# Kernel optimization log

Measured on AMD Instinct MI355X. Metric: run time of the kernel, lower is better.

## Reference

```python
import jax, jax.numpy as jnp
import numpy as np

B, N, P, K = 4, 512, 1024, 20
LMAX, SH_DIM, MUL, NB = 2, 9, 64, 20
CUT, T, NSPEC = 4.0, 3, 119
E = N * K
PE = P * K
L_SLICES = [(0, 1), (1, 4), (4, 9)]


def spherical_harmonics(vec):
    # component-normalized real SH up to l=2 on the unit vector (e3nn 'component' norm: ||Y_l||^2 = 2l+1)
    r = jnp.sqrt(jnp.sum(vec * vec, axis=-1, keepdims=True))
    u = vec / jnp.maximum(r, 1e-9)
    x, y, z = u[:, 0], u[:, 1], u[:, 2]
    s3, s5, s15 = 3.0 ** 0.5, 5.0 ** 0.5, 15.0 ** 0.5
    return jnp.stack([
        jnp.ones_like(x),
        s3 * x, s3 * y, s3 * z,
        s15 * x * y, s15 * y * z, 0.5 * s5 * (3.0 * z * z - 1.0),
        s15 * x * z, 0.5 * s15 * (x * x - y * y),
    ], axis=-1)  # [E, 9]


def radial_basis(r):
    # gaussian RBF, centers linspace(0, cutoff, num_basis)
    centers = jnp.linspace(0.0, CUT, NB)
    sigma = CUT / NB
    return jnp.exp(-((r[:, None] - centers[None, :]) / sigma) ** 2)


def per_l_linear(a, Wl):
    # a: [n, 9, mul]; Wl: [3, mul, mul]; independent channel-mixing per angular momentum l
    return jnp.concatenate([a[:, s:e, :] @ Wl[l] for l, (s, e) in enumerate(L_SLICES)], axis=1)


def conv_layer(h_src_feats, sh, rbf, src, dst, n_out, Wr1, br1, Wr2, br2, Wl, Wg):
    # radial MLP -> per-edge weights; gather scalar source features; tensor-product-style message sh (x) (w*s)
    w = jax.nn.silu(rbf @ Wr1 + br1) @ Wr2 + br2                 # [E, mul]
    s_src = h_src_feats[src, 0, :]                               # [E, mul]
    m = sh[:, :, None] * (s_src * w)[:, None, :]                 # [E, 9, mul]
    a = jax.ops.segment_sum(m, dst, num_segments=n_out) / (K ** 0.5)
    u = per_l_linear(a, Wl)                                      # [n, 9, mul]
    gate = jax.nn.sigmoid(a[:, 0, :] @ Wg)                       # gate activation for l>0
    return jnp.concatenate([jax.nn.silu(u[:, :1, :]), u[:, 1:, :] * gate[:, None, :]], axis=1)


def _forward(atom_xyz, atom_edges_displacement, cell, probe_xyz, probe_edges_displacement,
             W_embed, Wr1, br1, Wr2, br2, Wl, Wg,
             pWr1, pbr1, pWr2, pbr2, pWl, pWg, W_out,
             atom_edges, probe_edges, nodes):
    Na, Np, Et, PEt = B * N, B * P, B * E, B * PE
    pos = atom_xyz.reshape(Na, 3)          # unpad_and_cat with uniform lengths == reshape
    ppos = probe_xyz.reshape(Np, 3)
    node_off = (jnp.arange(B, dtype=atom_edges.dtype) * N)[:, None, None]
    a_edges = (atom_edges + node_off).reshape(Et, 2)
    p_off = jnp.concatenate([node_off, (jnp.arange(B, dtype=atom_edges.dtype) * P)[:, None, None]], axis=2)
    p_edges = (probe_edges + p_off).reshape(PEt, 2)
    # fractional displacement -> cartesian via per-graph cell (repeat_interleave over edges)
    cell_a = jnp.repeat(cell, E, axis=0)
    cell_p = jnp.repeat(cell, PE, axis=0)
    disp_a = jnp.einsum('ei,eij->ej', atom_edges_displacement.reshape(Et, 3), cell_a)
    disp_p = jnp.einsum('ei,eij->ej', probe_edges_displacement.reshape(PEt, 3), cell_p)
    src, dst = a_edges[:, 0], a_edges[:, 1]
    edge_vec = pos[dst] - (pos[src] + disp_a)
    sh = spherical_harmonics(edge_vec)
    rbf = radial_basis(jnp.linalg.norm(edge_vec, axis=1))
    psrc, pdst = p_edges[:, 0], p_edges[:, 1]
    p_vec = ppos[pdst] - (pos[psrc] + disp_p)
    psh = spherical_harmonics(p_vec)
    prbf = radial_basis(jnp.linalg.norm(p_vec, axis=1))
    # AtomicConfigurationModel: one-hot species -> scalar channel, T interaction layers, keep per-layer reps
    onehot = jax.nn.one_hot(nodes.reshape(Na), NSPEC, dtype=W_embed.dtype)
    h = jnp.zeros((Na, SH_DIM, MUL), W_embed.dtype).at[:, 0, :].set(onehot @ W_embed)
    reps = []
    for t in range(T):
        h = h + conv_layer(h, sh, rbf, src, dst, Na, Wr1[t], br1[t], Wr2[t], br2[t], Wl[t], Wg[t])
        reps.append(h)
    # AtomicPotentialModel: atom->probe message passing using per-layer atom representations
    p = jnp.zeros((Np, SH_DIM, MUL), W_embed.dtype)
    for t in range(T):
        p = p + conv_layer(reps[t], psh, prbf, psrc, pdst, Np, pWr1[t], pbr1[t], pWr2[t], pbr2[t], pWl[t], pWg[t])
    out = (p[:, 0, :] @ W_out)[:, 0].reshape(B, P)  # readout to 0e scalar, pad_and_stack == reshape
    return out


def setup_inputs():
    key = jax.random.key(0)
    ks = jax.random.split(key, 20)
    f32 = jnp.float32
    atom_xyz = jax.random.uniform(ks[0], (B, N, 3), f32) * 8.0
    probe_xyz = jax.random.uniform(ks[1], (B, P, 3), f32) * 8.0
    cell = jnp.tile(jnp.eye(3, dtype=f32)[None] * 8.0, (B, 1, 1))
    atom_edges = jax.random.randint(ks[2], (B, E, 2), 0, N, jnp.int32)
    probe_edges = jnp.concatenate([
        jax.random.randint(ks[3], (B, PE, 1), 0, N, jnp.int32),
        jax.random.randint(ks[4], (B, PE, 1), 0, P, jnp.int32)], axis=2)
    atom_edges_displacement = jax.random.randint(ks[5], (B, E, 3), -1, 2).astype(f32)
    probe_edges_displacement = jax.random.randint(ks[6], (B, PE, 3), -1, 2).astype(f32)
    nodes = jax.random.randint(ks[7], (B, N), 1, 84, jnp.int32)
    num_nodes = jnp.full((B,), N, jnp.int32)
    num_atom_edges = jnp.full((B,), E, jnp.int32)
    num_probes = jnp.full((B,), P, jnp.int32)
    num_probe_edges = jnp.full((B,), PE, jnp.int32)
    rn = lambda k, s: jax.random.normal(k, s, f32) * 0.1
    W_embed = rn(ks[8], (NSPEC, MUL))
    Wr1 = rn(ks[9], (T, NB, 100)); br1 = jnp.zeros((T, 100), f32)
    Wr2 = rn(ks[10], (T, 100, MUL)); br2 = jnp.zeros((T, MUL), f32)
    Wl = rn(ks[11], (T, 3, MUL, MUL)); Wg = rn(ks[12], (T, MUL, MUL))
    pWr1 = rn(ks[13], (T, NB, 100)); pbr1 = jnp.zeros((T, 100), f32)
    pWr2 = rn(ks[14], (T, 100, MUL)); pbr2 = jnp.zeros((T, MUL), f32)
    pWl = rn(ks[15], (T, 3, MUL, MUL)); pWg = rn(ks[16], (T, MUL, MUL))
    W_out = rn(ks[17], (MUL, 1))
    return dict(atom_xyz=atom_xyz, atom_edges_displacement=atom_edges_displacement, cell=cell,
                probe_xyz=probe_xyz, probe_edges_displacement=probe_edges_displacement,
                W_embed=W_embed, Wr1=Wr1, br1=br1, Wr2=Wr2, br2=br2, Wl=Wl, Wg=Wg,
                pWr1=pWr1, pbr1=pbr1, pWr2=pWr2, pbr2=pbr2, pWl=pWl, pWg=pWg, W_out=W_out,
                atom_edges=atom_edges, probe_edges=probe_edges, nodes=nodes,
                num_nodes=num_nodes, num_atom_edges=num_atom_edges,
                num_probes=num_probes, num_probe_edges=num_probe_edges)


def reference(atom_xyz, atom_edges_displacement, cell, probe_xyz, probe_edges_displacement,
              W_embed, Wr1, br1, Wr2, br2, Wl, Wg,
              pWr1, pbr1, pWr2, pbr2, pWl, pWg, W_out,
              atom_edges, probe_edges, nodes, num_nodes, num_atom_edges, num_probes, num_probe_edges):
    # num_* are uniform (all graphs same size); unpad_and_cat reduces to reshape.
    return _forward(atom_xyz, atom_edges_displacement, cell, probe_xyz, probe_edges_displacement,
                    W_embed, Wr1, br1, Wr2, br2, Wl, Wg,
                    pWr1, pbr1, pWr2, pbr2, pWl, pWg, W_out,
                    atom_edges, probe_edges, nodes)
```

## Files before the change

### kernel.cpp

```cpp
#include <hip/hip_runtime.h>
#include <math.h>

#define Bc 4
#define Nc 512
#define Pc 1024
#define Kc 20
#define MUL 64
#define NBc 20
#define HID 100
#define Tc 3
#define CUTc 4.0f
#define Ec (Nc * Kc)
#define PEc (Pc * Kc)
#define NA (Bc * Nc)
#define NP (Bc * Pc)
#define ET (Bc * Ec)
#define PET (Bc * PEc)
#define TBL 1024
#define RMAXT 5.25f
#define CAP 64
#define TROWS 8
#define TBLOCKS (6 * TBL / TROWS)
#define ZBLOCKS 8
#define EBLOCKS 32

__device__ __forceinline__ float silu_f(float x) { return x / (1.0f + __expf(-x)); }
__device__ __forceinline__ float lane_bcast_f(float v, int l) {
    return __int_as_float(__builtin_amdgcn_readlane(__float_as_int(v), l));
}

__global__ __launch_bounds__(256) void front_kernel(
    const float* __restrict__ Wr1, const float* __restrict__ pWr1,
    const float* __restrict__ br1, const float* __restrict__ pbr1,
    const float* __restrict__ Wr2, const float* __restrict__ pWr2,
    const float* __restrict__ br2, const float* __restrict__ pbr2,
    const int* __restrict__ nodes, const float* __restrict__ Wemb,
    int* __restrict__ cnt_both, float* __restrict__ h0row,
    float* __restrict__ wtab)
{
    __shared__ float Hs[TROWS * HID];
    int bid = blockIdx.x;
    int t = threadIdx.x;

    if (bid < TBLOCKS) {
        int grow0 = bid * TROWS;
        int ly = grow0 / TBL;
        int t3 = (ly < 3) ? ly : ly - 3;
        const float* w1 = ((ly < 3) ? Wr1 : pWr1) + (size_t)t3 * NBc * HID;
        const float* b1 = ((ly < 3) ? br1 : pbr1) + (size_t)t3 * HID;
        const float* w2 = ((ly < 3) ? Wr2 : pWr2) + (size_t)t3 * HID * MUL;
        const float* b2 = ((ly < 3) ? br2 : pbr2) + (size_t)t3 * MUL;
        const float step = CUTc / (NBc - 1);
        const float inv_sigma = (float)NBc / CUTc;

        for (int id = t; id < TROWS * HID; id += 256) {
            int il = id / HID, j = id - il * HID;
            float r = (float)(grow0 % TBL + il) * (RMAXT / (float)TBL);
            float s = b1[j];
#pragma unroll
            for (int k = 0; k < NBc; ++k) {
                float tt = (r - k * step) * inv_sigma;
                s = fmaf(__expf(-tt * tt), w1[k * HID + j], s);
            }
            Hs[id] = silu_f(s);
        }
        __syncthreads();

        int il0 = t >> 6, c = t & 63;
        for (int il = il0; il < TROWS; il += 4) {
            float acc = b2[c];
#pragma unroll 4
            for (int j = 0; j < HID; ++j)
                acc = fmaf(Hs[il * HID + j], w2[(size_t)j * MUL + c], acc);
            wtab[(size_t)(grow0 + il) * MUL + c] = acc;
        }
    } else if (bid < TBLOCKS + ZBLOCKS) {
        int idx = (bid - TBLOCKS) * 256 + t;
        for (int i = idx; i < NA + NP; i += ZBLOCKS * 256) cnt_both[i] = 0;
    } else {
        int idx = (bid - TBLOCKS - ZBLOCKS) * 256 + t;
        for (int i = idx; i < NA * MUL; i += EBLOCKS * 256) {
            int a = i >> 6, c = i & 63;
            h0row[i] = Wemb[nodes[a] * MUL + c];
        }
    }
}

__global__ void geom_kernel(const float* __restrict__ apos,
                            const float* __restrict__ ppos,
                            const int* __restrict__ a_edges,
                            const int* __restrict__ p_edges,
                            const float* __restrict__ a_disp,
                            const float* __restrict__ p_disp,
                            const float* __restrict__ cell,
                            int* __restrict__ cnt_a, int* __restrict__ cnt_p,
                            float* __restrict__ br_a, int* __restrict__ bs_a,
                            float* __restrict__ br_p, int* __restrict__ bs_p)
{
    int e = blockIdx.x * 256 + threadIdx.x;
    if (e >= ET + PET) return;
    const int* edges; const float* displ; const float* pdst;
    int* cnt; float* brout; int* bsout;
    int el, Eper, dst_stride;
    if (e < ET) {
        el = e; edges = a_edges; displ = a_disp; pdst = apos;
        Eper = Ec; dst_stride = Nc; cnt = cnt_a; brout = br_a; bsout = bs_a;
    } else {
        el = e - ET; edges = p_edges; displ = p_disp; pdst = ppos;
        Eper = PEc; dst_stride = Pc; cnt = cnt_p; brout = br_p; bsout = bs_p;
    }
    int b = el / Eper;
    int sg = edges[el * 2 + 0] + b * Nc;
    int dg = edges[el * 2 + 1] + b * dst_stride;
    const float* C = cell + b * 9;
    float d0 = displ[el * 3 + 0], d1 = displ[el * 3 + 1], d2 = displ[el * 3 + 2];
    float dx = d0 * C[0] + d1 * C[3] + d2 * C[6];
    float dy = d0 * C[1] + d1 * C[4] + d2 * C[7];
    float dz = d0 * C[2] + d1 * C[5] + d2 * C[8];
    float vx = pdst[dg * 3 + 0] - (apos[sg * 3 + 0] + dx);
    float vy = pdst[dg * 3 + 1] - (apos[sg * 3 + 1] + dy);
    float vz = pdst[dg * 3 + 2] - (apos[sg * 3 + 2] + dz);
    float r = sqrtf(vx * vx + vy * vy + vz * vz);
    int pos = atomicAdd(&cnt[dg], 1);
    if (pos < CAP) {
        brout[(size_t)dg * CAP + pos] = r;
        bsout[(size_t)dg * CAP + pos] = sg;
    }
}

__global__ __launch_bounds__(256) void layer_kernel(
    const float* __restrict__ hsrc,
    float* __restrict__ outb,
    const int* __restrict__ cnt,
    const float* __restrict__ brk, const int* __restrict__ bsk,
    const float* __restrict__ wtab,
    const float* __restrict__ Wl0)
{
    __shared__ float tile[4][64];
    int c = threadIdx.x & 63;
    int w = threadIdx.x >> 6;
    int n = blockIdx.x * 4 + w;

    int m = min(cnt[n], CAP);
    float rvec = 0.0f; int svec = 0;
    if (c < m) { rvec = brk[(size_t)n * CAP + c]; svec = bsk[(size_t)n * CAP + c]; }
    float acc = 0.0f;
    const float scale = (float)TBL / RMAXT;
#pragma unroll 4
    for (int p = 0; p < m; ++p) {
        float rr = lane_bcast_f(rvec, p);
        int sg = __builtin_amdgcn_readlane(svec, p);
        float x = fminf(rr * scale, (float)TBL - 1.001f);
        int i0 = (int)x;
        float f = x - (float)i0;
        const float* tp = wtab + (size_t)i0 * MUL;
        float w0 = tp[c];
        float w1 = tp[MUL + c];
        float wv = fmaf(w1 - w0, f, w0);
        acc = fmaf(hsrc[(size_t)sg * MUL + c], wv, acc);
    }
    acc *= 0.22360679774997896f;

    tile[w][c] = acc;
    float u = 0.0f;
#pragma unroll
    for (int k4 = 0; k4 < 16; ++k4) {
        float4 av = *(const float4*)&tile[w][k4 * 4];
        u = fmaf(av.x, Wl0[(k4 * 4 + 0) * 64 + c], u);
        u = fmaf(av.y, Wl0[(k4 * 4 + 1) * 64 + c], u);
        u = fmaf(av.z, Wl0[(k4 * 4 + 2) * 64 + c], u);
        u = fmaf(av.w, Wl0[(k4 * 4 + 3) * 64 + c], u);
    }
    outb[(size_t)n * MUL + c] = hsrc[(size_t)n * MUL + c] + silu_f(u);
}

__global__ __launch_bounds__(256) void probe3_kernel(
    const float* __restrict__ rep0, const float* __restrict__ rep1,
    const float* __restrict__ rep2,
    const int* __restrict__ cnt,
    const float* __restrict__ brk, const int* __restrict__ bsk,
    const float* __restrict__ wtab,
    const float* __restrict__ pWl,
    const float* __restrict__ Wout,
    float* __restrict__ out)
{
    __shared__ float tile[4][64];
    int c = threadIdx.x & 63;
    int w = threadIdx.x >> 6;
    int n = blockIdx.x * 4 + w;

    int m = min(cnt[n], CAP);
    float rvec = 0.0f; int svec = 0;
    if (c < m) { rvec = brk[(size_t)n * CAP + c]; svec = bsk[(size_t)n * CAP + c]; }
    float acc0 = 0.0f, acc1 = 0.0f, acc2 = 0.0f;
    const float scale = (float)TBL / RMAXT;
    const float* wt0 = wtab;
    const float* wt1 = wtab + (size_t)TBL * MUL;
    const float* wt2 = wtab + (size_t)2 * TBL * MUL;
#pragma unroll 2
    for (int p = 0; p < m; ++p) {
        float rr = lane_bcast_f(rvec, p);
        int sg = __builtin_amdgcn_readlane(svec, p);
        float x = fminf(rr * scale, (float)TBL - 1.001f);
        int i0 = (int)x;
        float f = x - (float)i0;
        size_t rowo = (size_t)i0 * MUL + c;
        float wv0 = fmaf(wt0[rowo + MUL] - wt0[rowo], f, wt0[rowo]);
        float wv1 = fmaf(wt1[rowo + MUL] - wt1[rowo], f, wt1[rowo]);
        float wv2 = fmaf(wt2[rowo + MUL] - wt2[rowo], f, wt2[rowo]);
        size_t so = (size_t)sg * MUL + c;
        acc0 = fmaf(rep0[so], wv0, acc0);
        acc1 = fmaf(rep1[so], wv1, acc1);
        acc2 = fmaf(rep2[so], wv2, acc2);
    }
    const float isk = 0.22360679774997896f;
    float res = 0.0f;
    float accs[3] = {acc0, acc1, acc2};
#pragma unroll
    for (int t = 0; t < 3; ++t) {
        tile[w][c] = accs[t] * isk;
        const float* W = pWl + (size_t)t * 3 * MUL * MUL;
        float u = 0.0f;
#pragma unroll
        for (int k4 = 0; k4 < 16; ++k4) {
            float4 av = *(const float4*)&tile[w][k4 * 4];
            u = fmaf(av.x, W[(k4 * 4 + 0) * 64 + c], u);
            u = fmaf(av.y, W[(k4 * 4 + 1) * 64 + c], u);
            u = fmaf(av.z, W[(k4 * 4 + 2) * 64 + c], u);
            u = fmaf(av.w, W[(k4 * 4 + 3) * 64 + c], u);
        }
        res += silu_f(u);
    }

    float v = res * Wout[c];
#pragma unroll
    for (int o = 32; o > 0; o >>= 1) v += __shfl_down(v, o, 64);
    if (c == 0) out[n] = v;
}

extern "C" void kernel_launch(void* const* d_in, const int* in_sizes, int n_in,
                              void* d_out, int out_size, void* d_ws, size_t ws_size,
                              hipStream_t stream)
{
    const float* atom_xyz  = (const float*)d_in[0];
    const float* a_disp    = (const float*)d_in[1];
    const float* cell      = (const float*)d_in[2];
    const float* probe_xyz = (const float*)d_in[3];
    const float* p_disp    = (const float*)d_in[4];
    const float* W_embed   = (const float*)d_in[5];
    const float* Wr1       = (const float*)d_in[6];
    const float* br1       = (const float*)d_in[7];
    const float* Wr2       = (const float*)d_in[8];
    const float* br2       = (const float*)d_in[9];
    const float* Wl        = (const float*)d_in[10];
    const float* pWr1      = (const float*)d_in[12];
    const float* pbr1      = (const float*)d_in[13];
    const float* pWr2      = (const float*)d_in[14];
    const float* pbr2      = (const float*)d_in[15];
    const float* pWl       = (const float*)d_in[16];
    const float* W_out     = (const float*)d_in[18];
    const int*   atom_edges  = (const int*)d_in[19];
    const int*   probe_edges = (const int*)d_in[20];
    const int*   nodes       = (const int*)d_in[21];
    float* out = (float*)d_out;

    char* w = (char*)d_ws;
    auto alloc = [&](size_t bytes) -> void* {
        void* r = (void*)w;
        w += (bytes + 255) & ~(size_t)255;
        return r;
    };
    int*   cnt_both = (int*)alloc((size_t)(NA + NP) * 4);
    int*   cnt_a  = cnt_both;
    int*   cnt_p  = cnt_both + NA;
    float* br_a   = (float*)alloc((size_t)NA * CAP * 4);
    int*   bs_a   = (int*)alloc((size_t)NA * CAP * 4);
    float* br_p   = (float*)alloc((size_t)NP * CAP * 4);
    int*   bs_p   = (int*)alloc((size_t)NP * CAP * 4);
    float* h0row  = (float*)alloc((size_t)NA * MUL * 4);
    float* rep0   = (float*)alloc((size_t)NA * MUL * 4);
    float* rep1   = (float*)alloc((size_t)NA * MUL * 4);
    float* rep2   = (float*)alloc((size_t)NA * MUL * 4);
    float* wtab   = (float*)alloc((size_t)6 * TBL * MUL * 4);

    front_kernel<<<TBLOCKS + ZBLOCKS + EBLOCKS, 256, 0, stream>>>(
        Wr1, pWr1, br1, pbr1, Wr2, pWr2, br2, pbr2,
        nodes, W_embed, cnt_both, h0row, wtab);

    geom_kernel<<<(ET + PET + 255) / 256, 256, 0, stream>>>(
        atom_xyz, probe_xyz, atom_edges, probe_edges, a_disp, p_disp, cell,
        cnt_a, cnt_p, br_a, bs_a, br_p, bs_p);

    const float* hprev = h0row;
    float* reps[3] = {rep0, rep1, rep2};
    for (int t = 0; t < Tc; ++t) {
        layer_kernel<<<NA / 4, 256, 0, stream>>>(
            hprev, reps[t], cnt_a, br_a, bs_a,
            wtab + (size_t)t * TBL * MUL,
            Wl + (size_t)t * 3 * MUL * MUL);
        hprev = reps[t];
    }

    probe3_kernel<<<NP / 4, 256, 0, stream>>>(
        rep0, rep1, rep2, cnt_p, br_p, bs_p,
        wtab + (size_t)3 * TBL * MUL, pWl, W_out, out);
}
```

Before: 77.30 us.

## Interleave per-layer probe convolutions with atom layer launches in a combined kernel

Replaces the separate atom layer kernels and the single three-layer probe kernel with one kernel that runs atom-layer blocks and probe-layer blocks side by side. Probe interaction t now runs in the same launch as atom layer t+1, so probe work fills the GPU while the atom chain proceeds. The probe results are accumulated across launches in a new per-probe buffer with a phase flag. This adds a global read and write of that buffer per probe, and it gives up the single probe pass that reused the same edge list for all three layers.

Result: no change. 76.82 us (-0.6%).

```diff
diff --git a/kernel.cpp b/kernel.cpp
--- a/kernel.cpp
+++ b/kernel.cpp
@@ -128,114 +128,98 @@
     }
 }
 
-__global__ __launch_bounds__(256) void layer_kernel(
-    const float* __restrict__ hsrc,
-    float* __restrict__ outb,
-    const int* __restrict__ cnt,
-    const float* __restrict__ brk, const int* __restrict__ bsk,
-    const float* __restrict__ wtab,
-    const float* __restrict__ Wl0)
+__global__ __launch_bounds__(256) void layer_probe_kernel(
+    const float* __restrict__ hsrc, float* __restrict__ outb,
+    const int* __restrict__ cnt_a,
+    const float* __restrict__ br_a, const int* __restrict__ bs_a,
+    const float* __restrict__ awt, const float* __restrict__ Wl0,
+    int atomBlocks,
+    const float* __restrict__ rept,
+    const int* __restrict__ cnt_p,
+    const float* __restrict__ br_p, const int* __restrict__ bs_p,
+    const float* __restrict__ pwt, const float* __restrict__ pWl0,
+    float* __restrict__ resbuf, const float* __restrict__ Wout,
+    float* __restrict__ out, int phase)
 {
     __shared__ float tile[4][64];
     int c = threadIdx.x & 63;
     int w = threadIdx.x >> 6;
-    int n = blockIdx.x * 4 + w;
-
-    int m = min(cnt[n], CAP);
-    float rvec = 0.0f; int svec = 0;
-    if (c < m) { rvec = brk[(size_t)n * CAP + c]; svec = bsk[(size_t)n * CAP + c]; }
-    float acc = 0.0f;
     const float scale = (float)TBL / RMAXT;
+    const float isk = 0.22360679774997896f;
+
+    if (blockIdx.x < (unsigned)atomBlocks) {
+        int n = blockIdx.x * 4 + w;
+        int m = min(cnt_a[n], CAP);
+        float rvec = 0.0f; int svec = 0;
+        if (c < m) { rvec = br_a[(size_t)n * CAP + c]; svec = bs_a[(size_t)n * CAP + c]; }
+        float acc = 0.0f;
 #pragma unroll 4
-    for (int p = 0; p < m; ++p) {
-        float rr = lane_bcast_f(rvec, p);
-        int sg = __builtin_amdgcn_readlane(svec, p);
-        float x = fminf(rr * scale, (float)TBL - 1.001f);
-        int i0 = (int)x;
-        float f = x - (float)i0;
-        const float* tp = wtab + (size_t)i0 * MUL;
-        float w0 = tp[c];
-        float w1 = tp[MUL + c];
-        float wv = fmaf(w1 - w0, f, w0);
-        acc = fmaf(hsrc[(size_t)sg * MUL + c], wv, acc);
-    }
-    acc *= 0.22360679774997896f;
-
-    tile[w][c] = acc;
-    float u = 0.0f;
-#pragma unroll
-    for (int k4 = 0; k4 < 16; ++k4) {
-        float4 av = *(const float4*)&tile[w][k4 * 4];
-        u = fmaf(av.x, Wl0[(k4 * 4 + 0) * 64 + c], u);
-        u = fmaf(av.y, Wl0[(k4 * 4 + 1) * 64 + c], u);
-        u = fmaf(av.z, Wl0[(k4 * 4 + 2) * 64 + c], u);
-        u = fmaf(av.w, Wl0[(k4 * 4 + 3) * 64 + c], u);
-    }
-    outb[(size_t)n * MUL + c] = hsrc[(size_t)n * MUL + c] + silu_f(u);
-}
-
-__global__ __launch_bounds__(256) void probe3_kernel(
-    const float* __restrict__ rep0, const float* __restrict__ rep1,
-    const float* __restrict__ rep2,
-    const int* __restrict__ cnt,
-    const float* __restrict__ brk, const int* __restrict__ bsk,
-    const float* __restrict__ wtab,
-    const float* __restrict__ pWl,
-    const float* __restrict__ Wout,
-    float* __restrict__ out)
-{
-    __shared__ float tile[4][64];
-    int c = threadIdx.x & 63;
-    int w = threadIdx.x >> 6;
-    int n = blockIdx.x * 4 + w;
-
-    int m = min(cnt[n], CAP);
-    float rvec = 0.0f; int svec = 0;
-    if (c < m) { rvec = brk[(size_t)n * CAP + c]; svec = bsk[(size_t)n * CAP + c]; }
-    float acc0 = 0.0f, acc1 = 0.0f, acc2 = 0.0f;
-    const float scale = (float)TBL / RMAXT;
-    const float* wt0 = wtab;
-    const float* wt1 = wtab + (size_t)TBL * MUL;
-    const float* wt2 = wtab + (size_t)2 * TBL * MUL;
-#pragma unroll 2
-    for (int p = 0; p < m; ++p) {
-        float rr = lane_bcast_f(rvec, p);
-        int sg = __builtin_amdgcn_readlane(svec, p);
-        float x = fminf(rr * scale, (float)TBL - 1.001f);
-        int i0 = (int)x;
-        float f = x - (float)i0;
-        size_t rowo = (size_t)i0 * MUL + c;
-        float wv0 = fmaf(wt0[rowo + MUL] - wt0[rowo], f, wt0[rowo]);
-        float wv1 = fmaf(wt1[rowo + MUL] - wt1[rowo], f, wt1[rowo]);
-        float wv2 = fmaf(wt2[rowo + MUL] - wt2[rowo], f, wt2[rowo]);
-        size_t so = (size_t)sg * MUL + c;
-        acc0 = fmaf(rep0[so], wv0, acc0);
-        acc1 = fmaf(rep1[so], wv1, acc1);
-        acc2 = fmaf(rep2[so], wv2, acc2);
-    }
-    const float isk = 0.22360679774997896f;
-    float res = 0.0f;
-    float accs[3] = {acc0, acc1, acc2};
-#pragma unroll
-    for (int t = 0; t < 3; ++t) {
-        tile[w][c] = accs[t] * isk;
-        const float* W = pWl + (size_t)t * 3 * MUL * MUL;
+        for (int p = 0; p < m; ++p) {
+            float rr = lane_bcast_f(rvec, p);
+            int sg = __builtin_amdgcn_readlane(svec, p);
+            float x = fminf(rr * scale, (float)TBL - 1.001f);
+            int i0 = (int)x;
+            float f = x - (float)i0;
+            const float* tp = awt + (size_t)i0 * MUL;
+            float w0 = tp[c];
+            float w1 = tp[MUL + c];
+            float wv = fmaf(w1 - w0, f, w0);
+            acc = fmaf(hsrc[(size_t)sg * MUL + c], wv, acc);
+        }
+        tile[w][c] = acc * isk;
         float u = 0.0f;
 #pragma unroll
         for (int k4 = 0; k4 < 16; ++k4) {
             float4 av = *(const float4*)&tile[w][k4 * 4];
-            u = fmaf(av.x, W[(k4 * 4 + 0) * 64 + c], u);
-            u = fmaf(av.y, W[(k4 * 4 + 1) * 64 + c], u);
-            u = fmaf(av.z, W[(k4 * 4 + 2) * 64 + c], u);
-            u = fmaf(av.w, W[(k4 * 4 + 3) * 64 + c], u);
-        }
-        res += silu_f(u);
+            u = fmaf(av.x, Wl0[(k4 * 4 + 0) * 64 + c], u);
+            u = fmaf(av.y, Wl0[(k4 * 4 + 1) * 64 + c], u);
+            u = fmaf(av.z, Wl0[(k4 * 4 + 2) * 64 + c], u);
+            u = fmaf(av.w, Wl0[(k4 * 4 + 3) * 64 + c], u);
+        }
+        outb[(size_t)n * MUL + c] = hsrc[(size_t)n * MUL + c] + silu_f(u);
+    } else {
+        int n = (blockIdx.x - atomBlocks) * 4 + w;
+        int m = min(cnt_p[n], CAP);
+        float rvec = 0.0f; int svec = 0;
+        if (c < m) { rvec = br_p[(size_t)n * CAP + c]; svec = bs_p[(size_t)n * CAP + c]; }
+        float acc = 0.0f;
+#pragma unroll 4
+        for (int p = 0; p < m; ++p) {
+            float rr = lane_bcast_f(rvec, p);
+            int sg = __builtin_amdgcn_readlane(svec, p);
+            float x = fminf(rr * scale, (float)TBL - 1.001f);
+            int i0 = (int)x;
+            float f = x - (float)i0;
+            const float* tp = pwt + (size_t)i0 * MUL;
+            float w0 = tp[c];
+            float w1 = tp[MUL + c];
+            float wv = fmaf(w1 - w0, f, w0);
+            acc = fmaf(rept[(size_t)sg * MUL + c], wv, acc);
+        }
+        tile[w][c] = acc * isk;
+        float u = 0.0f;
+#pragma unroll
+        for (int k4 = 0; k4 < 16; ++k4) {
+            float4 av = *(const float4*)&tile[w][k4 * 4];
+            u = fmaf(av.x, pWl0[(k4 * 4 + 0) * 64 + c], u);
+            u = fmaf(av.y, pWl0[(k4 * 4 + 1) * 64 + c], u);
+            u = fmaf(av.z, pWl0[(k4 * 4 + 2) * 64 + c], u);
+            u = fmaf(av.w, pWl0[(k4 * 4 + 3) * 64 + c], u);
+        }
+        float s = silu_f(u);
+        size_t idx = (size_t)n * MUL + c;
+        if (phase == 0) {
+            resbuf[idx] = s;
+        } else if (phase == 1) {
+            resbuf[idx] += s;
+        } else {
+            float res = resbuf[idx] + s;
+            float v = res * Wout[c];
+#pragma unroll
+            for (int o = 32; o > 0; o >>= 1) v += __shfl_down(v, o, 64);
+            if (c == 0) out[n] = v;
+        }
     }
-
-    float v = res * Wout[c];
-#pragma unroll
-    for (int o = 32; o > 0; o >>= 1) v += __shfl_down(v, o, 64);
-    if (c == 0) out[n] = v;
 }
 
 extern "C" void kernel_launch(void* const* d_in, const int* in_sizes, int n_in,
@@ -281,7 +265,12 @@
     float* rep0   = (float*)alloc((size_t)NA * MUL * 4);
     float* rep1   = (float*)alloc((size_t)NA * MUL * 4);
     float* rep2   = (float*)alloc((size_t)NA * MUL * 4);
+    float* resbuf = (float*)alloc((size_t)NP * MUL * 4);
     float* wtab   = (float*)alloc((size_t)6 * TBL * MUL * 4);
+    float* pwtab  = wtab + (size_t)3 * TBL * MUL;
+
+    const int AB = NA / 4;
+    const int PB = NP / 4;
 
     front_kernel<<<TBLOCKS + ZBLOCKS + EBLOCKS, 256, 0, stream>>>(
         Wr1, pWr1, br1, pbr1, Wr2, pWr2, br2, pbr2,
@@ -291,17 +280,25 @@
         atom_xyz, probe_xyz, atom_edges, probe_edges, a_disp, p_disp, cell,
         cnt_a, cnt_p, br_a, bs_a, br_p, bs_p);
 
-    const float* hprev = h0row;
-    float* reps[3] = {rep0, rep1, rep2};
-    for (int t = 0; t < Tc; ++t) {
-        layer_kernel<<<NA / 4, 256, 0, stream>>>(
-            hprev, reps[t], cnt_a, br_a, bs_a,
-            wtab + (size_t)t * TBL * MUL,
-            Wl + (size_t)t * 3 * MUL * MUL);
-        hprev = reps[t];
-    }
-
-    probe3_kernel<<<NP / 4, 256, 0, stream>>>(
-        rep0, rep1, rep2, cnt_p, br_p, bs_p,
-        wtab + (size_t)3 * TBL * MUL, pWl, W_out, out);
-}
+    layer_probe_kernel<<<AB, 256, 0, stream>>>(
+        h0row, rep0, cnt_a, br_a, bs_a, wtab, Wl,
+        AB,
+        nullptr, cnt_p, br_p, bs_p, nullptr, nullptr, resbuf, W_out, out, 0);
+
+    layer_probe_kernel<<<AB + PB, 256, 0, stream>>>(
+        rep0, rep1, cnt_a, br_a, bs_a, wtab + (size_t)TBL * MUL, Wl + (size_t)3 * MUL * MUL,
+        AB,
+        rep0, cnt_p, br_p, bs_p, pwtab, pWl, resbuf, W_out, out, 0);
+
+    layer_probe_kernel<<<AB + PB, 256, 0, stream>>>(
+        rep1, rep2, cnt_a, br_a, bs_a, wtab + (size_t)2 * TBL * MUL, Wl + (size_t)6 * MUL * MUL,
+        AB,
+        rep1, cnt_p, br_p, bs_p, pwtab + (size_t)TBL * MUL, pWl + (size_t)3 * MUL * MUL,
+        resbuf, W_out, out, 1);
+
+    layer_probe_kernel<<<PB, 256, 0, stream>>>(
+        nullptr, nullptr, cnt_a, br_a, bs_a, nullptr, nullptr,
+        0,
+        rep2, cnt_p, br_p, bs_p, pwtab + (size_t)2 * TBL * MUL, pWl + (size_t)6 * MUL * MUL,
+        resbuf, W_out, out, 2);
+}
```
